# Performance work log

Measured on AMD Instinct MI355X. Metric: run time of the kernel, lower is better.

The kernel has to match this reference:

```python
import jax, jax.numpy as jnp
import numpy as np

EPS = 1e-08
K = 3  # kernel size


def _conv_same_per_sample(xi, wi):
    # xi: [Cin,H,W], wi: [Cout,Cin,K,K] -> [Cout,H,W]
    out = jax.lax.conv_general_dilated(
        xi[None],  # [1,Cin,H,W]
        wi,
        window_strides=(1, 1),
        padding=((K // 2, K // 2), (K // 2, K // 2)),
        dimension_numbers=("NCHW", "OIHW", "NCHW"),
    )
    return out[0]


def setup_inputs() -> dict:
    key = jax.random.key(0)
    ks = jax.random.split(key, 6)
    B, Cin, Cout, S, H, W = 16, 256, 256, 512, 64, 64
    x = jax.random.normal(ks[0], (B, Cin, H, W), dtype=jnp.float32)
    y = jax.random.normal(ks[1], (B, S), dtype=jnp.float32)
    weights = jax.random.normal(ks[2], (Cout, Cin, K, K), dtype=jnp.float32)
    bias = jnp.zeros((Cout,), dtype=jnp.float32)
    # nn.Linear(style_channels, in_channels)
    lim = 1.0 / np.sqrt(S)
    style_w = jax.random.uniform(ks[3], (Cin, S), jnp.float32, -lim, lim)
    style_b = jax.random.uniform(ks[4], (Cin,), jnp.float32, -lim, lim)
    return {"x": x, "y": y, "weights": weights, "bias": bias,
            "style_w": style_w, "style_b": style_b}


def reference(x, y, weights, bias, style_w, style_b):
    # style: [B, Cin]
    style = y @ style_w.T + style_b
    # modulate: [B, Cout, Cin, K, K]
    w_mod = weights[None] * style[:, None, :, None, None]
    # demodulate over (Cin, K, K)
    w_std = jnp.sqrt(jnp.sum(w_mod * w_mod, axis=(2, 3, 4), keepdims=True) + EPS)
    w_demod = w_mod / w_std
    # per-sample conv (equivalent to groups=batch grouped conv)
    out = jax.vmap(_conv_same_per_sample)(x, w_demod)  # [B,Cout,H,W]
    return out + bias[None, :, None, None]
```

## Files before the change

kernel.cpp:

```cpp
#include <hip/hip_runtime.h>

typedef __bf16 bf16;
typedef __bf16 bf16x8 __attribute__((ext_vector_type(8)));
typedef float f32x4 __attribute__((ext_vector_type(4)));

#define EPS 1e-8f

constexpr int B = 16, CI = 256, CO = 256, S = 512, H = 64, W = 64;
constexpr int PH = 66;
constexpr int TAPS = 9;

constexpr size_t WS_WD    = 0;
constexpr size_t WS_XPAD  = 1179648;
constexpr size_t WS_STYLE = WS_XPAD + (size_t)B*PH*32*PH*16;
constexpr size_t WS_WSQT  = WS_STYLE + 16384;
constexpr size_t WS_INV   = WS_WSQT + 262144;

__global__ void prep1_kernel(const float* __restrict__ y,
                             const float* __restrict__ sw,
                             const float* __restrict__ sb,
                             const float* __restrict__ wts,
                             bf16x8* __restrict__ wd,
                             float* __restrict__ wsqT,
                             float* __restrict__ style) {
    __shared__ float t[8 * 289];
    int i = blockIdx.x;
    if (i < 256) {
        int cb = i & 31;
        int ib = i >> 5;
        const float* src = wts + ((size_t)cb * 8) * (CI * TAPS) + ib * 32 * TAPS;
        for (int e = threadIdx.x; e < 8 * 288; e += 256) {
            int col = e / 288, idx = e - col * 288;
            t[col * 289 + idx] = src[(size_t)col * (CI * TAPS) + idx];
        }
        __syncthreads();
        for (int c = threadIdx.x; c < 288; c += 256) {
            int co_l = c & 7, ci8_l = (c >> 3) & 3, tap = c >> 5;
            bf16x8 v;
#pragma unroll
            for (int j = 0; j < 8; ++j) v[j] = (bf16)t[co_l * 289 + (ci8_l * 8 + j) * 9 + tap];
            wd[((size_t)tap * 32 + ib * 4 + ci8_l) * CO + cb * 8 + co_l] = v;
        }
        int c = threadIdx.x;
        int co_l = c & 7, ci_l = c >> 3;
        float s = 0.f;
#pragma unroll
        for (int tap = 0; tap < 9; ++tap) {
            float w = t[co_l * 289 + ci_l * 9 + tap];
            s += w * w;
        }
        wsqT[((size_t)(ib * 32 + ci_l)) * CO + cb * 8 + co_l] = s;
    } else {
        int i2 = i - 256;
        int b = i2 >> 6;
        int c = (i2 & 63) * 4 + (threadIdx.x >> 6);
        int lane = threadIdx.x & 63;
        const float* yr = y + (size_t)b * S;
        const float* wr = sw + (size_t)c * S;
        float acc = 0.f;
#pragma unroll
        for (int k = 0; k < 8; ++k) acc += yr[lane + k * 64] * wr[lane + k * 64];
        for (int off = 32; off; off >>= 1) acc += __shfl_down(acc, off, 64);
        if (lane == 0) style[b * CI + c] = acc + sb[c];
    }
}

__global__ void prep2_kernel(const float* __restrict__ x,
                             const float* __restrict__ style,
                             const float* __restrict__ wsqT,
                             bf16x8* __restrict__ xp,
                             float* __restrict__ invstd) {
    __shared__ float t[4][32][W + 1];
    int i = blockIdx.x;
    if (i >= 2176) {
        int b = i - 2176, co = threadIdx.x;
        const float* st = style + b * CI;
        float acc = 0.f;
        for (int ci = 0; ci < CI; ++ci) {
            float s = st[ci];
            acc += wsqT[(size_t)ci * CO + co] * s * s;
        }
        invstd[b * CO + co] = rsqrtf(acc + EPS);
        return;
    }
    int cc = i & 7;
    int u = i >> 3;
    int yb = u % 17, b = u / 17;
    bf16x8 z;
#pragma unroll
    for (int j = 0; j < 8; ++j) z[j] = (bf16)0.f;

    if (yb == 16) {
        for (int q = threadIdx.x; q < 2 * 4 * PH; q += 256) {
            int row = (q >= 4 * PH) ? (PH - 1) : 0;
            int rest = (q >= 4 * PH) ? q - 4 * PH : q;
            int sub = rest / PH, col = rest - sub * PH;
            xp[(((size_t)b * PH + row) * 32 + cc * 4 + sub) * PH + col] = z;
        }
        return;
    }

    int h0 = yb * 4;
    const float* xb = x + ((size_t)b * CI + cc * 32) * (H * W);
    const float* st = style + b * CI + cc * 32;
#pragma unroll
    for (int k = 0; k < 8; ++k) {
        int idx = threadIdx.x + k * 256;
        int w4 = idx & 15, ci = (idx >> 4) & 31, r = idx >> 9;
        f32x4 v = *(const f32x4*)(xb + ((size_t)ci * H + h0 + r) * W + w4 * 4);
        float s = st[ci];
        t[r][ci][w4 * 4 + 0] = v.x * s;
        t[r][ci][w4 * 4 + 1] = v.y * s;
        t[r][ci][w4 * 4 + 2] = v.z * s;
        t[r][ci][w4 * 4 + 3] = v.w * s;
    }
    __syncthreads();
#pragma unroll
    for (int k = 0; k < 4; ++k) {
        int q = threadIdx.x + k * 256;
        int w = q & 63, sub = (q >> 6) & 3, r = q >> 8;
        bf16x8 v;
#pragma unroll
        for (int j = 0; j < 8; ++j) v[j] = (bf16)t[r][sub * 8 + j][w];
        xp[(((size_t)b * PH + h0 + r + 1) * 32 + cc * 4 + sub) * PH + (w + 1)] = v;
    }
    if (threadIdx.x < 32) {
        int r = threadIdx.x >> 3, sub = (threadIdx.x >> 1) & 3;
        int col = (threadIdx.x & 1) ? (PH - 1) : 0;
        xp[(((size_t)b * PH + h0 + r + 1) * 32 + cc * 4 + sub) * PH + col] = z;
    }
}

#define LOAD_TAP(c8_, kh_, kw_, av_, bv_)                                         \
    {                                                                             \
        const bf16x8* wq_ = wbase + ((size_t)((kh_)*3 + (kw_)) * 32 + (c8_)) * CO;\
        const bf16x8* xq_ = xbase + ((size_t)(kh_) * 32 * PH + (size_t)(c8_) * PH + (kw_)); \
        _Pragma("unroll") for (int a_ = 0; a_ < 4; ++a_) (av_)[a_] = wq_[a_ * 16];\
        _Pragma("unroll") for (int jr_ = 0; jr_ < 2; ++jr_)                       \
            _Pragma("unroll") for (int jc_ = 0; jc_ < 4; ++jc_)                   \
                (bv_)[jr_ * 4 + jc_] = xq_[(size_t)jr_ * 32 * PH + jc_ * 16];     \
    }

#define MFMA_STEP(av_, bv_)                                                       \
    _Pragma("unroll") for (int a_ = 0; a_ < 4; ++a_)                              \
        _Pragma("unroll") for (int j_ = 0; j_ < 8; ++j_)                          \
            acc[a_][j_] = __builtin_amdgcn_mfma_f32_16x16x32_bf16(                \
                (av_)[a_], (bv_)[j_], acc[a_][j_], 0, 0, 0);

__global__ __launch_bounds__(256, 2) void conv_kernel(
                            const bf16x8* __restrict__ wd,
                            const bf16x8* __restrict__ xp,
                            const float* __restrict__ bias,
                            const float* __restrict__ invstd,
                            float* __restrict__ out) {
    int i = blockIdx.x;
    int xcd = i & 7, t = i >> 3;
    int b = xcd * 2 + (t >> 5);
    int rest = t & 31;
    int cotile = rest & 1, rowquad = rest >> 1;
    int tid = threadIdx.x;
    int wave = tid >> 6, lane = tid & 63;
    int co_half = wave & 1, sp_half = wave >> 1;
    int r0 = rowquad * 4 + sp_half * 2;
    int co_base = cotile * 128 + co_half * 64;
    int lm = lane & 15, lk = lane >> 4;

    f32x4 acc[4][8] = {};

    const bf16x8* xpb = xp + (size_t)b * PH * 32 * PH;
    const bf16x8* wbase = wd + (size_t)lk * CO + co_base + lm;
    const bf16x8* xbase = xpb + ((size_t)r0 * 32 + lk) * PH + lm;

    bf16x8 av0[4], bv0[8], av1[4], bv1[8];

    LOAD_TAP(0, 0, 0, av0, bv0);

#pragma unroll 1
    for (int c8a = 0; c8a < 32; c8a += 8) {
#pragma unroll
        for (int v = 0; v < 18; ++v) {
            const int ntap = (v + 1) % 9;
            const int nkh = ntap / 3, nkw = ntap % 3;
            int nc8 = (v == 17) ? ((c8a + 8) & 31)
                                : (c8a + ((v + 1) / 9) * 4);
            if ((v & 1) == 0) {
                LOAD_TAP(nc8, nkh, nkw, av1, bv1);
                __builtin_amdgcn_sched_barrier(0);
                MFMA_STEP(av0, bv0);
            } else {
                LOAD_TAP(nc8, nkh, nkw, av0, bv0);
                __builtin_amdgcn_sched_barrier(0);
                MFMA_STEP(av1, bv1);
            }
        }
    }

#pragma unroll
    for (int a = 0; a < 4; ++a) {
#pragma unroll
        for (int g = 0; g < 4; ++g) {
            int co = co_base + a * 16 + lk * 4 + g;
            float sc = invstd[b * CO + co];
            float bvl = bias[co];
#pragma unroll
            for (int jr = 0; jr < 2; ++jr) {
                size_t o = (((size_t)b * CO + co) * H + r0 + jr) * W;
#pragma unroll
                for (int jc = 0; jc < 4; ++jc)
                    out[o + jc * 16 + lm] = acc[a][jr * 4 + jc][g] * sc + bvl;
            }
        }
    }
}

extern "C" void kernel_launch(void* const* d_in, const int* in_sizes, int n_in,
                              void* d_out, int out_size, void* d_ws, size_t ws_size,
                              hipStream_t stream) {
    const float* x    = (const float*)d_in[0];
    const float* y    = (const float*)d_in[1];
    const float* wts  = (const float*)d_in[2];
    const float* bias = (const float*)d_in[3];
    const float* sw   = (const float*)d_in[4];
    const float* sb   = (const float*)d_in[5];
    float* out = (float*)d_out;

    char* ws = (char*)d_ws;
    bf16x8* wd    = (bf16x8*)(ws + WS_WD);
    bf16x8* xpad  = (bf16x8*)(ws + WS_XPAD);
    float* style  = (float*)(ws + WS_STYLE);
    float* wsqT   = (float*)(ws + WS_WSQT);
    float* invstd = (float*)(ws + WS_INV);

    prep1_kernel<<<dim3(1280), dim3(256), 0, stream>>>(y, sw, sb, wts, wd, wsqT, style);
    prep2_kernel<<<dim3(2192), dim3(256), 0, stream>>>(x, style, wsqT, xpad, invstd);
    conv_kernel<<<dim3(512), dim3(256), 0, stream>>>(wd, xpad, bias, invstd, out);
}
```

Baseline: 191.2 us.

## Rewrite input padding prep without LDS transpose, unroll invstd, raise MFMA priority

The x-pad/modulate stage now has each thread read 8 channels of one pixel directly and write one packed bf16x8, replacing the shared-memory transpose with a flat grid of 8192 blocks. Border zeroing moves to separate blocks. The invstd reduction caches squared style in LDS and uses eight independent accumulators. The conv MFMA block is also wrapped in s_setprio so waves issuing MFMAs get higher priority. The direct loads are coalesced per channel but strided across channels, which risks lower load efficiency than the previous float4 path.

```diff
diff --git a/kernel.cpp b/kernel.cpp
--- a/kernel.cpp
+++ b/kernel.cpp
@@ -70,65 +70,66 @@
                              const float* __restrict__ wsqT,
                              bf16x8* __restrict__ xp,
                              float* __restrict__ invstd) {
-    __shared__ float t[4][32][W + 1];
+    __shared__ float st2[256];
     int i = blockIdx.x;
-    if (i >= 2176) {
-        int b = i - 2176, co = threadIdx.x;
-        const float* st = style + b * CI;
-        float acc = 0.f;
-        for (int ci = 0; ci < CI; ++ci) {
-            float s = st[ci];
-            acc += wsqT[(size_t)ci * CO + co] * s * s;
-        }
-        invstd[b * CO + co] = rsqrtf(acc + EPS);
+    if (i < 8192) {
+        int b = i >> 9, rem = i & 511;
+        int ci8 = rem & 31;
+        int row = ((rem >> 5) << 2) + (threadIdx.x >> 6);
+        int col = threadIdx.x & 63;
+        const float* xb = x + (((size_t)b * CI + ci8 * 8) * H + row) * W + col;
+        const float* st = style + b * CI + ci8 * 8;
+        bf16x8 v;
+#pragma unroll
+        for (int j = 0; j < 8; ++j) v[j] = (bf16)(xb[(size_t)j * H * W] * st[j]);
+        xp[(((size_t)b * PH + row + 1) * 32 + ci8) * PH + col + 1] = v;
         return;
     }
-    int cc = i & 7;
-    int u = i >> 3;
-    int yb = u % 17, b = u / 17;
-    bf16x8 z;
-#pragma unroll
-    for (int j = 0; j < 8; ++j) z[j] = (bf16)0.f;
-
-    if (yb == 16) {
-        for (int q = threadIdx.x; q < 2 * 4 * PH; q += 256) {
-            int row = (q >= 4 * PH) ? (PH - 1) : 0;
-            int rest = (q >= 4 * PH) ? q - 4 * PH : q;
-            int sub = rest / PH, col = rest - sub * PH;
-            xp[(((size_t)b * PH + row) * 32 + cc * 4 + sub) * PH + col] = z;
+    if (i < 8448) {
+        int bi = i - 8192;
+        int b = bi >> 4, part = bi & 15;
+        bf16x8 z;
+#pragma unroll
+        for (int j = 0; j < 8; ++j) z[j] = (bf16)0.f;
+        for (int t = threadIdx.x; t < 520; t += 256) {
+            int idx = part * 520 + t;
+            int row, ci8, col;
+            if (idx < 4224) {
+                int rowsel = idx / 2112;
+                int rem = idx - rowsel * 2112;
+                row = rowsel ? (PH - 1) : 0;
+                ci8 = rem / 66;
+                col = rem - ci8 * 66;
+            } else {
+                int j2 = idx - 4224;
+                int colsel = j2 >> 11;
+                int rem = j2 & 2047;
+                row = 1 + (rem >> 5);
+                ci8 = rem & 31;
+                col = colsel ? (PH - 1) : 0;
+            }
+            xp[(((size_t)b * PH + row) * 32 + ci8) * PH + col] = z;
         }
         return;
     }
-
-    int h0 = yb * 4;
-    const float* xb = x + ((size_t)b * CI + cc * 32) * (H * W);
-    const float* st = style + b * CI + cc * 32;
-#pragma unroll
-    for (int k = 0; k < 8; ++k) {
-        int idx = threadIdx.x + k * 256;
-        int w4 = idx & 15, ci = (idx >> 4) & 31, r = idx >> 9;
-        f32x4 v = *(const f32x4*)(xb + ((size_t)ci * H + h0 + r) * W + w4 * 4);
-        float s = st[ci];
-        t[r][ci][w4 * 4 + 0] = v.x * s;
-        t[r][ci][w4 * 4 + 1] = v.y * s;
-        t[r][ci][w4 * 4 + 2] = v.z * s;
-        t[r][ci][w4 * 4 + 3] = v.w * s;
-    }
+    int b = i - 8448, co = threadIdx.x;
+    float s = style[b * CI + co];
+    st2[co] = s * s;
     __syncthreads();
-#pragma unroll
-    for (int k = 0; k < 4; ++k) {
-        int q = threadIdx.x + k * 256;
-        int w = q & 63, sub = (q >> 6) & 3, r = q >> 8;
-        bf16x8 v;
-#pragma unroll
-        for (int j = 0; j < 8; ++j) v[j] = (bf16)t[r][sub * 8 + j][w];
-        xp[(((size_t)b * PH + h0 + r + 1) * 32 + cc * 4 + sub) * PH + (w + 1)] = v;
-    }
-    if (threadIdx.x < 32) {
-        int r = threadIdx.x >> 3, sub = (threadIdx.x >> 1) & 3;
-        int col = (threadIdx.x & 1) ? (PH - 1) : 0;
-        xp[(((size_t)b * PH + h0 + r + 1) * 32 + cc * 4 + sub) * PH + col] = z;
-    }
+    float a0 = 0.f, a1 = 0.f, a2 = 0.f, a3 = 0.f;
+    float a4 = 0.f, a5 = 0.f, a6 = 0.f, a7 = 0.f;
+    for (int ci = 0; ci < CI; ci += 8) {
+        a0 += wsqT[(size_t)(ci + 0) * CO + co] * st2[ci + 0];
+        a1 += wsqT[(size_t)(ci + 1) * CO + co] * st2[ci + 1];
+        a2 += wsqT[(size_t)(ci + 2) * CO + co] * st2[ci + 2];
+        a3 += wsqT[(size_t)(ci + 3) * CO + co] * st2[ci + 3];
+        a4 += wsqT[(size_t)(ci + 4) * CO + co] * st2[ci + 4];
+        a5 += wsqT[(size_t)(ci + 5) * CO + co] * st2[ci + 5];
+        a6 += wsqT[(size_t)(ci + 6) * CO + co] * st2[ci + 6];
+        a7 += wsqT[(size_t)(ci + 7) * CO + co] * st2[ci + 7];
+    }
+    float acc = ((a0 + a1) + (a2 + a3)) + ((a4 + a5) + (a6 + a7));
+    invstd[b * CO + co] = rsqrtf(acc + EPS);
 }
 
 #define LOAD_TAP(c8_, kh_, kw_, av_, bv_)                                         \
@@ -142,10 +143,12 @@
     }
 
 #define MFMA_STEP(av_, bv_)                                                       \
+    __builtin_amdgcn_s_setprio(1);                                                \
     _Pragma("unroll") for (int a_ = 0; a_ < 4; ++a_)                              \
         _Pragma("unroll") for (int j_ = 0; j_ < 8; ++j_)                          \
             acc[a_][j_] = __builtin_amdgcn_mfma_f32_16x16x32_bf16(                \
-                (av_)[a_], (bv_)[j_], acc[a_][j_], 0, 0, 0);
+                (av_)[a_], (bv_)[j_], acc[a_][j_], 0, 0, 0);                      \
+    __builtin_amdgcn_s_setprio(0);
 
 __global__ __launch_bounds__(256, 2) void conv_kernel(
                             const bf16x8* __restrict__ wd,
@@ -232,6 +235,6 @@
     float* invstd = (float*)(ws + WS_INV);
 
     prep1_kernel<<<dim3(1280), dim3(256), 0, stream>>>(y, sw, sb, wts, wd, wsqT, style);
-    prep2_kernel<<<dim3(2192), dim3(256), 0, stream>>>(x, style, wsqT, xpad, invstd);
+    prep2_kernel<<<dim3(8464), dim3(256), 0, stream>>>(x, style, wsqT, xpad, invstd);
     conv_kernel<<<dim3(512), dim3(256), 0, stream>>>(wd, xpad, bias, invstd, out);
 }
```

Result: no change. 191.8 us (+0.3%).

## Split prep2 into smaller row tiles, unroll invstd reduction, add MFMA priority hints

Applied to the files above, without the earlier changes.

The modulate-and-pad kernel now handles two rows per block instead of four, roughly doubling the block count to spread the x-conversion traffic across more CUs. The invstd path stages squared style values in shared memory and uses eight independent accumulators to break the serial FMA chain. The conv kernel wraps each MFMA burst in s_setprio raises so a wave keeps issue priority during its matrix block. The extra blocks add launch and index overhead, and the priority hints may change how waves interleave loads with MFMAs.

```diff
diff --git a/kernel.cpp b/kernel.cpp
--- a/kernel.cpp
+++ b/kernel.cpp
@@ -70,28 +70,39 @@
                              const float* __restrict__ wsqT,
                              bf16x8* __restrict__ xp,
                              float* __restrict__ invstd) {
-    __shared__ float t[4][32][W + 1];
+    __shared__ float t[2][32][W + 1];
     int i = blockIdx.x;
-    if (i >= 2176) {
-        int b = i - 2176, co = threadIdx.x;
-        const float* st = style + b * CI;
-        float acc = 0.f;
-        for (int ci = 0; ci < CI; ++ci) {
-            float s = st[ci];
-            acc += wsqT[(size_t)ci * CO + co] * s * s;
-        }
+    int tid = threadIdx.x;
+    if (i >= 4224) {
+        int b = i - 4224, co = tid;
+        float* tf = &t[0][0][0];
+        float s = style[b * CI + co];
+        tf[co] = s * s;
+        __syncthreads();
+        float a0 = 0.f, a1 = 0.f, a2 = 0.f, a3 = 0.f;
+        float a4 = 0.f, a5 = 0.f, a6 = 0.f, a7 = 0.f;
+        for (int ci = 0; ci < CI; ci += 8) {
+            a0 += wsqT[(size_t)(ci + 0) * CO + co] * tf[ci + 0];
+            a1 += wsqT[(size_t)(ci + 1) * CO + co] * tf[ci + 1];
+            a2 += wsqT[(size_t)(ci + 2) * CO + co] * tf[ci + 2];
+            a3 += wsqT[(size_t)(ci + 3) * CO + co] * tf[ci + 3];
+            a4 += wsqT[(size_t)(ci + 4) * CO + co] * tf[ci + 4];
+            a5 += wsqT[(size_t)(ci + 5) * CO + co] * tf[ci + 5];
+            a6 += wsqT[(size_t)(ci + 6) * CO + co] * tf[ci + 6];
+            a7 += wsqT[(size_t)(ci + 7) * CO + co] * tf[ci + 7];
+        }
+        float acc = ((a0 + a1) + (a2 + a3)) + ((a4 + a5) + (a6 + a7));
         invstd[b * CO + co] = rsqrtf(acc + EPS);
         return;
     }
-    int cc = i & 7;
-    int u = i >> 3;
-    int yb = u % 17, b = u / 17;
     bf16x8 z;
 #pragma unroll
     for (int j = 0; j < 8; ++j) z[j] = (bf16)0.f;
 
-    if (yb == 16) {
-        for (int q = threadIdx.x; q < 2 * 4 * PH; q += 256) {
+    if (i >= 4096) {
+        int j2 = i - 4096;
+        int cc = j2 & 7, b = j2 >> 3;
+        for (int q = tid; q < 2 * 4 * PH; q += 256) {
             int row = (q >= 4 * PH) ? (PH - 1) : 0;
             int rest = (q >= 4 * PH) ? q - 4 * PH : q;
             int sub = rest / PH, col = rest - sub * PH;
@@ -99,13 +110,15 @@
         }
         return;
     }
-
-    int h0 = yb * 4;
+    int cc = i & 7;
+    int u = i >> 3;
+    int rp = u & 31, b = u >> 5;
+    int h0 = rp * 2;
     const float* xb = x + ((size_t)b * CI + cc * 32) * (H * W);
     const float* st = style + b * CI + cc * 32;
 #pragma unroll
-    for (int k = 0; k < 8; ++k) {
-        int idx = threadIdx.x + k * 256;
+    for (int k = 0; k < 4; ++k) {
+        int idx = tid + k * 256;
         int w4 = idx & 15, ci = (idx >> 4) & 31, r = idx >> 9;
         f32x4 v = *(const f32x4*)(xb + ((size_t)ci * H + h0 + r) * W + w4 * 4);
         float s = st[ci];
@@ -116,17 +129,17 @@
     }
     __syncthreads();
 #pragma unroll
-    for (int k = 0; k < 4; ++k) {
-        int q = threadIdx.x + k * 256;
+    for (int k = 0; k < 2; ++k) {
+        int q = tid + k * 256;
         int w = q & 63, sub = (q >> 6) & 3, r = q >> 8;
         bf16x8 v;
 #pragma unroll
         for (int j = 0; j < 8; ++j) v[j] = (bf16)t[r][sub * 8 + j][w];
         xp[(((size_t)b * PH + h0 + r + 1) * 32 + cc * 4 + sub) * PH + (w + 1)] = v;
     }
-    if (threadIdx.x < 32) {
-        int r = threadIdx.x >> 3, sub = (threadIdx.x >> 1) & 3;
-        int col = (threadIdx.x & 1) ? (PH - 1) : 0;
+    if (tid < 16) {
+        int r = (tid >> 3) & 1, sub = (tid >> 1) & 3;
+        int col = (tid & 1) ? (PH - 1) : 0;
         xp[(((size_t)b * PH + h0 + r + 1) * 32 + cc * 4 + sub) * PH + col] = z;
     }
 }
@@ -142,10 +155,12 @@
     }
 
 #define MFMA_STEP(av_, bv_)                                                       \
+    __builtin_amdgcn_s_setprio(1);                                                \
     _Pragma("unroll") for (int a_ = 0; a_ < 4; ++a_)                              \
         _Pragma("unroll") for (int j_ = 0; j_ < 8; ++j_)                          \
             acc[a_][j_] = __builtin_amdgcn_mfma_f32_16x16x32_bf16(                \
-                (av_)[a_], (bv_)[j_], acc[a_][j_], 0, 0, 0);
+                (av_)[a_], (bv_)[j_], acc[a_][j_], 0, 0, 0);                      \
+    __builtin_amdgcn_s_setprio(0);
 
 __global__ __launch_bounds__(256, 2) void conv_kernel(
                             const bf16x8* __restrict__ wd,
@@ -154,9 +169,9 @@
                             const float* __restrict__ invstd,
                             float* __restrict__ out) {
     int i = blockIdx.x;
-    int xcd = i & 7, t = i >> 3;
-    int b = xcd * 2 + (t >> 5);
-    int rest = t & 31;
+    int xcd = i & 7, tq = i >> 3;
+    int b = xcd * 2 + (tq >> 5);
+    int rest = tq & 31;
     int cotile = rest & 1, rowquad = rest >> 1;
     int tid = threadIdx.x;
     int wave = tid >> 6, lane = tid & 63;
@@ -232,6 +247,6 @@
     float* invstd = (float*)(ws + WS_INV);
 
     prep1_kernel<<<dim3(1280), dim3(256), 0, stream>>>(y, sw, sb, wts, wd, wsqT, style);
-    prep2_kernel<<<dim3(2192), dim3(256), 0, stream>>>(x, style, wsqT, xpad, invstd);
+    prep2_kernel<<<dim3(4240), dim3(256), 0, stream>>>(x, style, wsqT, xpad, invstd);
     conv_kernel<<<dim3(512), dim3(256), 0, stream>>>(wd, xpad, bias, invstd, out);
 }
```

Result: no change. 190.5 us (-0.4%).
